# Performance work log

Measured on AMD Instinct MI355X. Metric: run time of the kernel, lower is better.

## Reference

```python
import jax, jax.numpy as jnp
import numpy as np

B, T, C = 4, 2048, 1024
H, D = 16, 64
EPS = 1.1920929e-07  # torch.finfo(float32).eps, used by F.rms_norm default


def setup_inputs() -> dict:
    key = jax.random.key(0)
    ks = jax.random.split(key, 6)
    x = jax.random.normal(ks[0], (B, T, C), dtype=jnp.float32)
    # rotary cache: theta = 10000^(-2i/D), broadcastable [1, T, 1, D//2]
    inv_freq = 1.0 / (10000.0 ** (jnp.arange(0, D // 2, dtype=jnp.float32) * 2.0 / D))
    ang = jnp.arange(T, dtype=jnp.float32)[:, None] * inv_freq[None, :]  # [T, D//2]
    cos = jnp.cos(ang)[None, :, None, :]
    sin = jnp.sin(ang)[None, :, None, :]
    s = 0.02
    Wq = jax.random.normal(ks[1], (C, C), dtype=jnp.float32) * s
    Wk = jax.random.normal(ks[2], (C, C), dtype=jnp.float32) * s
    Wv = jax.random.normal(ks[3], (C, C), dtype=jnp.float32) * s
    Wo = jax.random.normal(ks[4], (C, C), dtype=jnp.float32) * s
    return {"x": x, "cos": cos, "sin": sin, "Wq": Wq, "Wk": Wk, "Wv": Wv, "Wo": Wo}


def _rope(x, cos, sin):
    d = x.shape[-1] // 2
    x1, x2 = x[..., :d], x[..., d:]
    return jnp.concatenate([x1 * cos + x2 * sin, -x1 * sin + x2 * cos], axis=-1)


def _rmsnorm(x):
    ms = jnp.mean(jnp.square(x), axis=-1, keepdims=True)
    return x * jax.lax.rsqrt(ms + EPS)


def reference(x, cos, sin, Wq, Wk, Wv, Wo):
    Bx, Tx, Cx = x.shape
    q = (x @ Wq.T).reshape(Bx, Tx, H, D)
    k = (x @ Wk.T).reshape(Bx, Tx, H, D)
    v = (x @ Wv.T).reshape(Bx, Tx, H, D)
    q = _rmsnorm(_rope(q, cos, sin))
    k = _rmsnorm(_rope(k, cos, sin))
    scale = 1.0 / jnp.sqrt(jnp.float32(D))
    # non-causal SDPA
    scores = jnp.einsum('bthd,bshd->bhts', q, k) * scale  # [B,H,T,T]
    attn = jax.nn.softmax(scores, axis=-1)
    y = jnp.einsum('bhts,bshd->bthd', attn, v).reshape(Bx, Tx, Cx)
    return y @ Wo.T
```

## Files before the change

### kernel.cpp

```cpp
#include <hip/hip_runtime.h>

#define B_ 4
#define T_ 2048
#define C_ 1024
#define H_ 16
#define D_ 64
#define EPS_ 1.1920929e-07f

typedef __attribute__((ext_vector_type(8))) short bf16x8;
typedef __attribute__((ext_vector_type(4))) float f32x4;
typedef unsigned short u16;
typedef unsigned int u32;

__device__ inline u16 f2bf(float f) {
  unsigned u = __float_as_uint(f);
  unsigned r = (u + 0x7fffu + ((u >> 16) & 1u)) >> 16;
  return (u16)r;
}

__global__ __launch_bounds__(256) void cvt_bf16(const float* __restrict__ src,
                                                u16* __restrict__ dst, int n) {
  const int i = (blockIdx.x * 256 + threadIdx.x) * 4;
  if (i < n) {
    float4 v = *(const float4*)&src[i];
    ushort4 o;
    o.x = f2bf(v.x); o.y = f2bf(v.y); o.z = f2bf(v.z); o.w = f2bf(v.w);
    *(ushort4*)&dst[i] = o;
  }
}

__global__ __launch_bounds__(256) void cvt_weights(const float* __restrict__ wq,
                                                   const float* __restrict__ wk,
                                                   const float* __restrict__ wv,
                                                   const float* __restrict__ wo,
                                                   u16* __restrict__ wqkv,
                                                   u16* __restrict__ wob, int n) {
  const int i = (blockIdx.x * 256 + threadIdx.x) * 4;
  const int t = blockIdx.y;
  const float* src = (t == 0) ? wq : (t == 1) ? wk : (t == 2) ? wv : wo;
  u16* dst = (t == 3) ? wob : (wqkv + (size_t)t * n);
  if (i < n) {
    float4 v = *(const float4*)&src[i];
    ushort4 o;
    o.x = f2bf(v.x); o.y = f2bf(v.y); o.z = f2bf(v.z); o.w = f2bf(v.w);
    *(ushort4*)&dst[i] = o;
  }
}

__global__ __launch_bounds__(256) void gemm_qkv(const u16* __restrict__ X,
                                                const u16* __restrict__ W,
                                                u16* __restrict__ qb,
                                                u16* __restrict__ kb,
                                                u16* __restrict__ vb,
                                                const float* __restrict__ cs,
                                                const float* __restrict__ sn,
                                                int M, int K) {
  __shared__ short As[128 * 64];
  __shared__ short Bs[128 * 64];
  const int tid = threadIdx.x;
  const int lane = tid & 63;
  const int w = tid >> 6;
  const int wr = w >> 1, wc = w & 1;
  const int m0 = blockIdx.y * 128, n0 = blockIdx.x * 128;
  const int srow = lane >> 3;
  const int scol = (lane & 7) * 8;

  f32x4 acc[4][4];
#pragma unroll
  for (int mi = 0; mi < 4; ++mi)
#pragma unroll
    for (int ni = 0; ni < 4; ++ni)
      acc[mi][ni] = (f32x4){0.f, 0.f, 0.f, 0.f};

  const int r = lane & 15;
  const int quad = lane >> 4;

  bf16x8 av[4], bv[4];
#pragma unroll
  for (int i = 0; i < 4; ++i) {
    const int row = w * 32 + i * 8 + srow;
    av[i] = *(const bf16x8*)&X[(size_t)(m0 + row) * K + scol];
    bv[i] = *(const bf16x8*)&W[(size_t)(n0 + row) * K + scol];
  }

  for (int kt = 0; kt < K; kt += 64) {
#pragma unroll
    for (int i = 0; i < 4; ++i) {
      const int row = w * 32 + i * 8 + srow;
      *(bf16x8*)&As[row * 64 + scol] = av[i];
      *(bf16x8*)&Bs[row * 64 + scol] = bv[i];
    }
    __syncthreads();
    if (kt + 64 < K) {
#pragma unroll
      for (int i = 0; i < 4; ++i) {
        const int row = w * 32 + i * 8 + srow;
        av[i] = *(const bf16x8*)&X[(size_t)(m0 + row) * K + kt + 64 + scol];
        bv[i] = *(const bf16x8*)&W[(size_t)(n0 + row) * K + kt + 64 + scol];
      }
    }
#pragma unroll
    for (int kc = 0; kc < 2; ++kc) {
      const int ko = kc * 32 + quad * 8;
      bf16x8 a[4], b[4];
#pragma unroll
      for (int mi = 0; mi < 4; ++mi)
        a[mi] = *(const bf16x8*)&As[(wr * 64 + mi * 16 + r) * 64 + ko];
#pragma unroll
      for (int ni = 0; ni < 4; ++ni)
        b[ni] = *(const bf16x8*)&Bs[(wc * 64 + ni * 16 + r) * 64 + ko];
#pragma unroll
      for (int mi = 0; mi < 4; ++mi)
#pragma unroll
        for (int ni = 0; ni < 4; ++ni)
          acc[mi][ni] = __builtin_amdgcn_mfma_f32_16x16x32_bf16(a[mi], b[ni], acc[mi][ni], 0, 0, 0);
    }
    __syncthreads();
  }

  const int which = blockIdx.x >> 3;
  const int c0 = (blockIdx.x & 7) * 128 + wc * 64;
  u16* dst = (which == 0) ? qb : (which == 1) ? kb : vb;

  if (which < 2) {
#pragma unroll
    for (int mi = 0; mi < 4; ++mi)
#pragma unroll
      for (int j = 0; j < 4; ++j) {
        const int gr = m0 + wr * 64 + mi * 16 + quad * 4 + j;
        const int t = gr & (T_ - 1);
        float o[4];
#pragma unroll
        for (int ni = 0; ni < 2; ++ni) {
          const float c = cs[t * 32 + ni * 16 + r];
          const float s = sn[t * 32 + ni * 16 + r];
          const float x1 = acc[mi][ni][j], x2 = acc[mi][ni + 2][j];
          o[ni]     = x1 * c + x2 * s;
          o[ni + 2] = x2 * c - x1 * s;
        }
        float sq = o[0] * o[0] + o[1] * o[1] + o[2] * o[2] + o[3] * o[3];
        sq += __shfl_xor(sq, 1, 64);
        sq += __shfl_xor(sq, 2, 64);
        sq += __shfl_xor(sq, 4, 64);
        sq += __shfl_xor(sq, 8, 64);
        float rn = rsqrtf(sq * (1.0f / 64.0f) + EPS_);
        if (which == 0) rn *= 0.125f;
#pragma unroll
        for (int ni = 0; ni < 4; ++ni)
          dst[(size_t)gr * C_ + c0 + ni * 16 + r] = f2bf(o[ni] * rn);
      }
  } else {
#pragma unroll
    for (int mi = 0; mi < 4; ++mi)
#pragma unroll
      for (int ni = 0; ni < 4; ++ni) {
        const int gc = c0 + ni * 16 + r;
#pragma unroll
        for (int j = 0; j < 4; ++j) {
          const int gr = m0 + wr * 64 + mi * 16 + quad * 4 + j;
          dst[(size_t)gr * C_ + gc] = f2bf(acc[mi][ni][j]);
        }
      }
  }
}

__global__ __launch_bounds__(256) void gemm_out(const u16* __restrict__ X,
                                                const u16* __restrict__ W,
                                                float* __restrict__ Y,
                                                int M, int N, int K) {
  __shared__ short As[128 * 64];
  __shared__ short Bs[128 * 64];
  const int tid = threadIdx.x;
  const int lane = tid & 63;
  const int w = tid >> 6;
  const int wr = w >> 1, wc = w & 1;
  const int m0 = blockIdx.y * 128, n0 = blockIdx.x * 128;
  const int srow = lane >> 3;
  const int scol = (lane & 7) * 8;

  f32x4 acc[4][4];
#pragma unroll
  for (int mi = 0; mi < 4; ++mi)
#pragma unroll
    for (int ni = 0; ni < 4; ++ni)
      acc[mi][ni] = (f32x4){0.f, 0.f, 0.f, 0.f};

  const int r = lane & 15;
  const int quad = lane >> 4;

  bf16x8 av[4], bv[4];
#pragma unroll
  for (int i = 0; i < 4; ++i) {
    const int row = w * 32 + i * 8 + srow;
    av[i] = *(const bf16x8*)&X[(size_t)(m0 + row) * K + scol];
    bv[i] = *(const bf16x8*)&W[(size_t)(n0 + row) * K + scol];
  }

  for (int kt = 0; kt < K; kt += 64) {
#pragma unroll
    for (int i = 0; i < 4; ++i) {
      const int row = w * 32 + i * 8 + srow;
      *(bf16x8*)&As[row * 64 + scol] = av[i];
      *(bf16x8*)&Bs[row * 64 + scol] = bv[i];
    }
    __syncthreads();
    if (kt + 64 < K) {
#pragma unroll
      for (int i = 0; i < 4; ++i) {
        const int row = w * 32 + i * 8 + srow;
        av[i] = *(const bf16x8*)&X[(size_t)(m0 + row) * K + kt + 64 + scol];
        bv[i] = *(const bf16x8*)&W[(size_t)(n0 + row) * K + kt + 64 + scol];
      }
    }
#pragma unroll
    for (int kc = 0; kc < 2; ++kc) {
      const int ko = kc * 32 + quad * 8;
      bf16x8 a[4], b[4];
#pragma unroll
      for (int mi = 0; mi < 4; ++mi)
        a[mi] = *(const bf16x8*)&As[(wr * 64 + mi * 16 + r) * 64 + ko];
#pragma unroll
      for (int ni = 0; ni < 4; ++ni)
        b[ni] = *(const bf16x8*)&Bs[(wc * 64 + ni * 16 + r) * 64 + ko];
#pragma unroll
      for (int mi = 0; mi < 4; ++mi)
#pragma unroll
        for (int ni = 0; ni < 4; ++ni)
          acc[mi][ni] = __builtin_amdgcn_mfma_f32_16x16x32_bf16(a[mi], b[ni], acc[mi][ni], 0, 0, 0);
    }
    __syncthreads();
  }

#pragma unroll
  for (int mi = 0; mi < 4; ++mi)
#pragma unroll
    for (int ni = 0; ni < 4; ++ni) {
      const int gc = n0 + wc * 64 + ni * 16 + r;
#pragma unroll
      for (int j = 0; j < 4; ++j) {
        const int gr = m0 + wr * 64 + mi * 16 + quad * 4 + j;
        Y[(size_t)gr * N + gc] = acc[mi][ni][j];
      }
    }
}

__global__ __launch_bounds__(256) void flash_mfma(const u16* __restrict__ Qb,
                                                  const u16* __restrict__ Kb,
                                                  const u16* __restrict__ Vb,
                                                  u16* __restrict__ Yb) {
  __shared__ u16 Ks[64][72];
  __shared__ u16 Vt[64][72];
  __shared__ u16 Ps[128][72];
  const int tid = threadIdx.x;
  const int lane = tid & 63;
  const int w = tid >> 6;
  const int r = lane & 15;
  const int quad = lane >> 4;
  const int qt = blockIdx.x, bh = blockIdx.y;
  const int b = bh >> 4, h = bh & 15;
  const int srow = lane;
  const int sd0 = w * 16;
  const int vslot = (srow & 15) * 4 + (srow >> 4);

  {
    const int row = tid >> 1, half = tid & 1;
    const size_t g = ((size_t)((b * T_ + qt * 128 + row) * H_ + h)) * D_ + half * 32;
    *(bf16x8*)&Ps[row][half * 32]      = *(const bf16x8*)&Qb[g];
    *(bf16x8*)&Ps[row][half * 32 + 8]  = *(const bf16x8*)&Qb[g + 8];
    *(bf16x8*)&Ps[row][half * 32 + 16] = *(const bf16x8*)&Qb[g + 16];
    *(bf16x8*)&Ps[row][half * 32 + 24] = *(const bf16x8*)&Qb[g + 24];
  }
  __syncthreads();
  bf16x8 qf[2][2];
#pragma unroll
  for (int qg = 0; qg < 2; ++qg)
#pragma unroll
    for (int kc = 0; kc < 2; ++kc)
      qf[qg][kc] = *(const bf16x8*)&Ps[w * 32 + qg * 16 + r][kc * 32 + quad * 8];

  f32x4 oacc[2][4];
#pragma unroll
  for (int qg = 0; qg < 2; ++qg)
#pragma unroll
    for (int ni = 0; ni < 4; ++ni) oacc[qg][ni] = (f32x4){0.f, 0.f, 0.f, 0.f};
  float l_i[2][4];
#pragma unroll
  for (int qg = 0; qg < 2; ++qg)
#pragma unroll
    for (int j = 0; j < 4; ++j) l_i[qg][j] = 0.f;

  bf16x8 k0, k1, v0, v1;
  {
    const size_t g = ((size_t)((b * T_ + srow) * H_ + h)) * D_ + sd0;
    k0 = *(const bf16x8*)&Kb[g];
    k1 = *(const bf16x8*)&Kb[g + 8];
    v0 = *(const bf16x8*)&Vb[g];
    v1 = *(const bf16x8*)&Vb[g + 8];
  }

  for (int kt = 0; kt < T_; kt += 64) {
    *(bf16x8*)&Ks[srow][sd0] = k0;
    *(bf16x8*)&Ks[srow][sd0 + 8] = k1;
#pragma unroll
    for (int i = 0; i < 8; ++i) Vt[sd0 + i][vslot] = (u16)v0[i];
#pragma unroll
    for (int i = 0; i < 8; ++i) Vt[sd0 + 8 + i][vslot] = (u16)v1[i];
    __syncthreads();
    if (kt + 64 < T_) {
      const size_t g = ((size_t)((b * T_ + kt + 64 + srow) * H_ + h)) * D_ + sd0;
      k0 = *(const bf16x8*)&Kb[g];
      k1 = *(const bf16x8*)&Kb[g + 8];
      v0 = *(const bf16x8*)&Vb[g];
      v1 = *(const bf16x8*)&Vb[g + 8];
    }

#pragma unroll
    for (int qg = 0; qg < 2; ++qg) {
      f32x4 s[4];
#pragma unroll
      for (int ni = 0; ni < 4; ++ni) {
        s[ni] = (f32x4){0.f, 0.f, 0.f, 0.f};
#pragma unroll
        for (int kc = 0; kc < 2; ++kc) {
          bf16x8 kf = *(const bf16x8*)&Ks[ni * 16 + r][kc * 32 + quad * 8];
          s[ni] = __builtin_amdgcn_mfma_f32_16x16x32_bf16(qf[qg][kc], kf, s[ni], 0, 0, 0);
        }
      }
#pragma unroll
      for (int j = 0; j < 4; ++j) {
        const float p0 = __expf(s[0][j]);
        const float p1 = __expf(s[1][j]);
        const float p2 = __expf(s[2][j]);
        const float p3 = __expf(s[3][j]);
        l_i[qg][j] += (p0 + p1) + (p2 + p3);
        const int prow = w * 32 + qg * 16 + quad * 4 + j;
        u32 lo = (u32)f2bf(p0) | ((u32)f2bf(p1) << 16);
        u32 hi = (u32)f2bf(p2) | ((u32)f2bf(p3) << 16);
        uint2 pk = make_uint2(lo, hi);
        *(uint2*)&Ps[prow][r * 4] = pk;
      }
#pragma unroll
      for (int kc = 0; kc < 2; ++kc) {
        bf16x8 pf = *(const bf16x8*)&Ps[w * 32 + qg * 16 + r][kc * 32 + quad * 8];
#pragma unroll
        for (int ni = 0; ni < 4; ++ni) {
          bf16x8 vf = *(const bf16x8*)&Vt[ni * 16 + r][kc * 32 + quad * 8];
          oacc[qg][ni] = __builtin_amdgcn_mfma_f32_16x16x32_bf16(pf, vf, oacc[qg][ni], 0, 0, 0);
        }
      }
    }
    __syncthreads();
  }

#pragma unroll
  for (int qg = 0; qg < 2; ++qg)
#pragma unroll
    for (int j = 0; j < 4; ++j) {
      float l = l_i[qg][j];
      l += __shfl_xor(l, 1, 64);
      l += __shfl_xor(l, 2, 64);
      l += __shfl_xor(l, 4, 64);
      l += __shfl_xor(l, 8, 64);
      const float inv = 1.0f / l;
      const int t = qt * 128 + w * 32 + qg * 16 + quad * 4 + j;
      const size_t gbase = ((size_t)((b * T_ + t) * H_ + h)) * D_;
#pragma unroll
      for (int ni = 0; ni < 4; ++ni)
        Yb[gbase + ni * 16 + r] = f2bf(oacc[qg][ni][j] * inv);
    }
}

extern "C" void kernel_launch(void* const* d_in, const int* in_sizes, int n_in,
                              void* d_out, int out_size, void* d_ws, size_t ws_size,
                              hipStream_t stream) {
  const float* x    = (const float*)d_in[0];
  const float* cosb = (const float*)d_in[1];
  const float* sinb = (const float*)d_in[2];
  const float* Wq   = (const float*)d_in[3];
  const float* Wk   = (const float*)d_in[4];
  const float* Wv   = (const float*)d_in[5];
  const float* Wo   = (const float*)d_in[6];
  float* out = (float*)d_out;

  const size_t NE = (size_t)B_ * T_ * C_;
  const int CC = C_ * C_;
  u16* xb   = (u16*)d_ws;
  u16* qb   = xb + NE;
  u16* kb   = qb + NE;
  u16* vb   = kb + NE;
  u16* wqkv = vb + NE;
  u16* wob  = wqkv + 3 * (size_t)CC;
  u16* yb   = xb;

  const int M = B_ * T_;

  cvt_bf16<<<(int)(NE / 1024), 256, 0, stream>>>(x, xb, (int)NE);
  dim3 wg(CC / 1024, 4);
  cvt_weights<<<wg, 256, 0, stream>>>(Wq, Wk, Wv, Wo, wqkv, wob, CC);

  dim3 qg(24, M / 128), gb(256);
  gemm_qkv<<<qg, gb, 0, stream>>>(xb, wqkv, qb, kb, vb, cosb, sinb, M, C_);

  dim3 fg(T_ / 128, B_ * H_);
  flash_mfma<<<fg, 256, 0, stream>>>(qb, kb, vb, yb);

  dim3 og(C_ / 128, M / 128);
  gemm_out<<<og, gb, 0, stream>>>(yb, wob, out, M, C_, C_);
}
```

Measured before the change: 337.2 us.

## Fold log2e into Q scale, use exp2, truncate P to bf16, shrink LDS

Multiplies the Q scale by log2(e) so the flash kernel can use exp2f instead of __expf. P is converted to bf16 by truncation rather than round-to-nearest-even. Q fragments are loaded straight from global memory into registers, which removes the LDS staging and one barrier. The P scratch buffer is halved by reusing per-wave rows across qg iterations. Truncating P adds a small bias in precision, and reusing the P rows across qg iterations relies on the per-wave ordering of LDS writes and reads.

```diff
diff --git a/kernel.cpp b/kernel.cpp
--- a/kernel.cpp
+++ b/kernel.cpp
@@ -6,6 +6,7 @@
 #define H_ 16
 #define D_ 64
 #define EPS_ 1.1920929e-07f
+#define QSCALE 0.18033688f
 
 typedef __attribute__((ext_vector_type(8))) short bf16x8;
 typedef __attribute__((ext_vector_type(4))) float f32x4;
@@ -144,7 +145,7 @@
         sq += __shfl_xor(sq, 4, 64);
         sq += __shfl_xor(sq, 8, 64);
         float rn = rsqrtf(sq * (1.0f / 64.0f) + EPS_);
-        if (which == 0) rn *= 0.125f;
+        if (which == 0) rn *= QSCALE;
 #pragma unroll
         for (int ni = 0; ni < 4; ++ni)
           dst[(size_t)gr * C_ + c0 + ni * 16 + r] = f2bf(o[ni] * rn);
@@ -250,7 +251,7 @@
                                                   u16* __restrict__ Yb) {
   __shared__ u16 Ks[64][72];
   __shared__ u16 Vt[64][72];
-  __shared__ u16 Ps[128][72];
+  __shared__ u16 Ps[64][72];
   const int tid = threadIdx.x;
   const int lane = tid & 63;
   const int w = tid >> 6;
@@ -262,21 +263,14 @@
   const int sd0 = w * 16;
   const int vslot = (srow & 15) * 4 + (srow >> 4);
 
-  {
-    const int row = tid >> 1, half = tid & 1;
-    const size_t g = ((size_t)((b * T_ + qt * 128 + row) * H_ + h)) * D_ + half * 32;
-    *(bf16x8*)&Ps[row][half * 32]      = *(const bf16x8*)&Qb[g];
-    *(bf16x8*)&Ps[row][half * 32 + 8]  = *(const bf16x8*)&Qb[g + 8];
-    *(bf16x8*)&Ps[row][half * 32 + 16] = *(const bf16x8*)&Qb[g + 16];
-    *(bf16x8*)&Ps[row][half * 32 + 24] = *(const bf16x8*)&Qb[g + 24];
-  }
-  __syncthreads();
   bf16x8 qf[2][2];
 #pragma unroll
-  for (int qg = 0; qg < 2; ++qg)
+  for (int qg = 0; qg < 2; ++qg) {
+    const size_t g = ((size_t)((b * T_ + qt * 128 + w * 32 + qg * 16 + r) * H_ + h)) * D_;
 #pragma unroll
     for (int kc = 0; kc < 2; ++kc)
-      qf[qg][kc] = *(const bf16x8*)&Ps[w * 32 + qg * 16 + r][kc * 32 + quad * 8];
+      qf[qg][kc] = *(const bf16x8*)&Qb[g + kc * 32 + quad * 8];
+  }
 
   f32x4 oacc[2][4];
 #pragma unroll
@@ -328,20 +322,19 @@
       }
 #pragma unroll
       for (int j = 0; j < 4; ++j) {
-        const float p0 = __expf(s[0][j]);
-        const float p1 = __expf(s[1][j]);
-        const float p2 = __expf(s[2][j]);
-        const float p3 = __expf(s[3][j]);
+        const float p0 = exp2f(s[0][j]);
+        const float p1 = exp2f(s[1][j]);
+        const float p2 = exp2f(s[2][j]);
+        const float p3 = exp2f(s[3][j]);
         l_i[qg][j] += (p0 + p1) + (p2 + p3);
-        const int prow = w * 32 + qg * 16 + quad * 4 + j;
-        u32 lo = (u32)f2bf(p0) | ((u32)f2bf(p1) << 16);
-        u32 hi = (u32)f2bf(p2) | ((u32)f2bf(p3) << 16);
-        uint2 pk = make_uint2(lo, hi);
-        *(uint2*)&Ps[prow][r * 4] = pk;
+        const u32 lo = (__float_as_uint(p0) >> 16) | (__float_as_uint(p1) & 0xffff0000u);
+        const u32 hi = (__float_as_uint(p2) >> 16) | (__float_as_uint(p3) & 0xffff0000u);
+        const int prow = w * 16 + quad * 4 + j;
+        *(uint2*)&Ps[prow][r * 4] = make_uint2(lo, hi);
       }
 #pragma unroll
       for (int kc = 0; kc < 2; ++kc) {
-        bf16x8 pf = *(const bf16x8*)&Ps[w * 32 + qg * 16 + r][kc * 32 + quad * 8];
+        bf16x8 pf = *(const bf16x8*)&Ps[w * 16 + r][kc * 32 + quad * 8];
 #pragma unroll
         for (int ni = 0; ni < 4; ++ni) {
           bf16x8 vf = *(const bf16x8*)&Vt[ni * 16 + r][kc * 32 + quad * 8];
```

New measurement: 349.0 us. 1.03x slower.
